# Kernel tuning notes

Hardware: AMD Instinct MI355X
Metric: run time of the kernel (lower is better)

## Reference

```python
import jax, jax.numpy as jnp
import numpy as np

T = 3
R = 0.05  # threshold on SQUARED distance (as in the source: dis < r)
N, M = 4, 384

_PSPEC = [("hW1", (3, 64)), ("hb1", (64,)), ("hW2", (64, 128)), ("hb2", (128,)), ("hW3", (128, 3)), ("hb3", (3,)),
          ("fW1", (6, 64)), ("fb1", (64,)), ("fW2", (64, 128)), ("fb2", (128,)), ("fW3", (128, 128)), ("fb3", (128,)),
          ("gW1", (128, 64)), ("gb1", (64,)), ("gW2", (64, 32)), ("gb2", (32,)), ("gW3", (32, 3)), ("gb3", (3,))]


def setup_inputs() -> dict:
    key = jax.random.key(0)
    inp = {"x": jax.random.uniform(key, (N, M, 3), jnp.float32)}
    for i, (name, shp) in enumerate(_PSPEC):
        k = jax.random.fold_in(key, i + 1)
        scale = 1.0 / np.sqrt(shp[0]) if len(shp) == 2 else 0.01
        inp[name] = jax.random.normal(k, (T,) + shp, jnp.float32) * jnp.float32(scale)
    return inp


def _mlp(x, W1, b1, W2, b2, W3, b3, final_relu):
    h = jax.nn.relu(x @ W1 + b1)
    h = jax.nn.relu(h @ W2 + b2)
    o = h @ W3 + b3
    return jax.nn.relu(o) if final_relu else o


def _forward(x, hW1, hb1, hW2, hb2, hW3, hb3, fW1, fb1, fW2, fb2, fW3, fb3, gW1, gb1, gW2, gb2, gW3, gb3):
    n, m, _ = x.shape
    diff = x[:, :, None, :] - x[:, None, :, :]              # (N,M,M,3)
    adj = jnp.sum(diff * diff, axis=-1) < R                 # (N,M,M) squared-dist ball
    state = x
    for t in range(T):
        # NOTE on MLP_h / delta: in the source, xj and xi inside getTimeEdges are
        # IDENTICAL broadcasts of xi_delta (both x.unsqueeze(-2).repeat over dim -2),
        # so xi[adj] = xj[adj] - xi[adj] == 0 everywhere. The relative-position
        # slot is therefore exactly zeros and delta = MLP_h(state) never affects
        # the output (and receives zero gradient in torch as well).
        rel = jnp.zeros((n, m, m, 3), x.dtype)
        # state[n,i,j,:] = state[n,j,:] where adj[n,i,j], else 0
        sfull = jnp.where(adj[..., None], state[:, None, :, :], 0.0)  # (N,M,M,3)
        eij = jnp.concatenate([rel, sfull], axis=-1)                   # (N,M,M,6)
        e = _mlp(eij, fW1[t], fb1[t], fW2[t], fb2[t], fW3[t], fb3[t], True)  # (N,M,M,128)
        e = jnp.where(adj[..., None], e, 0.0)
        agg = jnp.max(e, axis=2)                                       # max over neighbors j -> (N,M,128)
        state = _mlp(agg, gW1[t], gb1[t], gW2[t], gb2[t], gW3[t], gb3[t], True) + state
    return state


def reference(x, hW1, hb1, hW2, hb2, hW3, hb3, fW1, fb1, fW2, fb2, fW3, fb3, gW1, gb1, gW2, gb2, gW3, gb3):
    return _forward(x, hW1, hb1, hW2, hb2, hW3, hb3, fW1, fb1, fW2, fb2, fW3, fb3, gW1, gb1, gW2, gb2, gW3, gb3)
```

## Files before the change

### kernel.cpp

```cpp
#include <hip/hip_runtime.h>

#define MNODES 384
#define RTHRESH 0.05f
#define NWAVES 6
#define NBLOCKS 256


__device__ __forceinline__ void phi_stage(
    const float* __restrict__ fW1, const float* __restrict__ fb1,
    const float* __restrict__ fW2, const float* __restrict__ fb2,
    const float* __restrict__ fW3, const float* __restrict__ fb3,
    float s0, float s1, float s2, int lane,
    float* __restrict__ H1, float* __restrict__ H2,
    float* __restrict__ phidst )
{
    float v = fb1[lane];
    v = fmaf(s0, fW1[3 * 64 + lane], v);
    v = fmaf(s1, fW1[4 * 64 + lane], v);
    v = fmaf(s2, fW1[5 * 64 + lane], v);
    H1[lane] = fmaxf(v, 0.0f);

    const int l2 = lane * 2;
    const float2 b2 = *(const float2*)(fb2 + l2);
    float a0 = b2.x, a1 = b2.y;
#pragma unroll 16
    for (int c = 0; c < 64; ++c) {
        const float h = H1[c];
        const float2 w = *(const float2*)(fW2 + c * 128 + l2);
        a0 = fmaf(h, w.x, a0);
        a1 = fmaf(h, w.y, a1);
    }
    H2[l2] = fmaxf(a0, 0.0f);
    H2[l2 + 1] = fmaxf(a1, 0.0f);

    const float2 b3 = *(const float2*)(fb3 + l2);
    float c0 = b3.x, c1 = b3.y;
#pragma unroll 16
    for (int c = 0; c < 128; ++c) {
        const float h = H2[c];
        const float2 w = *(const float2*)(fW3 + c * 128 + l2);
        c0 = fmaf(h, w.x, c0);
        c1 = fmaf(h, w.y, c1);
    }
    *(float2*)(phidst + l2) = make_float2(fmaxf(c0, 0.0f), fmaxf(c1, 0.0f));
}

__global__ __launch_bounds__(384) void adj_phi0_kernel(
    const float* __restrict__ x,
    const float* __restrict__ fW1, const float* __restrict__ fb1,
    const float* __restrict__ fW2, const float* __restrict__ fb2,
    const float* __restrict__ fW3, const float* __restrict__ fb3,
    int* __restrict__ cnt, unsigned short* __restrict__ lists,
    float* __restrict__ phiA)
{
    __shared__ float xs[MNODES * 3];
    __shared__ float work[NWAVES][192];
    const int tid = threadIdx.x;
    const int wv = tid >> 6, lane = tid & 63;
    const int node = blockIdx.x * NWAVES + wv;
    const int n = blockIdx.x >> 6;
    const int i = node - n * MNODES;

    for (int idx = tid; idx < MNODES * 3; idx += 384)
        xs[idx] = x[n * MNODES * 3 + idx];
    __syncthreads();

    const float s0 = xs[i * 3], s1 = xs[i * 3 + 1], s2 = xs[i * 3 + 2];
    unsigned short* ml = lists + (size_t)node * MNODES;
    int nc = 0;
#pragma unroll
    for (int rep = 0; rep < 6; ++rep) {
        const int j = rep * 64 + lane;
        float dx = xs[j * 3] - s0;
        float dy = xs[j * 3 + 1] - s1;
        float dz = xs[j * 3 + 2] - s2;
        float d2 = __fadd_rn(__fadd_rn(__fmul_rn(dx, dx), __fmul_rn(dy, dy)),
                             __fmul_rn(dz, dz));
        const bool a = d2 < RTHRESH;
        const unsigned long long m = __ballot(a);
        if (a) ml[nc + __popcll(m & ((1ull << lane) - 1ull))] = (unsigned short)j;
        nc += (int)__popcll(m);
    }
    if (lane == 0) cnt[node] = nc;

    phi_stage(fW1, fb1, fW2, fb2, fW3, fb3, s0, s1, s2, lane,
              &work[wv][0], &work[wv][64], phiA + (size_t)node * 128);
}

__global__ __launch_bounds__(384) void step_kernel(
    const float* __restrict__ phisrc, float* __restrict__ phidst,
    const int* __restrict__ cnt, const unsigned short* __restrict__ lists,
    const float* __restrict__ statesrc, float* __restrict__ statedst,
    const float* __restrict__ gW1, const float* __restrict__ gb1,
    const float* __restrict__ gW2, const float* __restrict__ gb2,
    const float* __restrict__ gW3, const float* __restrict__ gb3,
    const float* __restrict__ fW1n, const float* __restrict__ fb1n,
    const float* __restrict__ fW2n, const float* __restrict__ fb2n,
    const float* __restrict__ fW3n, const float* __restrict__ fb3n,
    int do_phi)
{
    __shared__ float work[NWAVES][224];
    const int tid = threadIdx.x;
    const int wv = tid >> 6, lane = tid & 63;
    const int node = __builtin_amdgcn_readfirstlane(blockIdx.x * NWAVES + wv);
    const int nbase = (blockIdx.x >> 6) * MNODES;
    const int nc = cnt[node];
    const unsigned short* ml = lists + (size_t)node * MNODES;
    const float* pb = phisrc + (size_t)nbase * 128;
    float* const aggL = &work[wv][0];
    float* const h1L  = &work[wv][128];
    float* const h2L  = &work[wv][192];
    const int l2 = lane * 2;

    float m[8], p[8];
#pragma unroll
    for (int k = 0; k < 8; ++k) { m[k] = 0.0f; p[k] = 0.0f; }
    const int last = nc - 1;
    for (int jj = 0; jj < nc; jj += 8) {
        const float* r[8];
#pragma unroll
        for (int k = 0; k < 8; ++k) {
            const int jc = jj + k;
            const int j = ml[jc < last ? jc : last];
            r[k] = pb + (size_t)j * 128;
        }
#pragma unroll
        for (int k = 0; k < 8; ++k) {
            const float2 v = *(const float2*)(r[k] + l2);
            m[k] = fmaxf(m[k], v.x);
            p[k] = fmaxf(p[k], v.y);
        }
    }
    aggL[l2] = fmaxf(fmaxf(fmaxf(m[0], m[1]), fmaxf(m[2], m[3])),
                     fmaxf(fmaxf(m[4], m[5]), fmaxf(m[6], m[7])));
    aggL[l2 + 1] = fmaxf(fmaxf(fmaxf(p[0], p[1]), fmaxf(p[2], p[3])),
                         fmaxf(fmaxf(p[4], p[5]), fmaxf(p[6], p[7])));

    float h = gb1[lane];
#pragma unroll 16
    for (int c = 0; c < 128; ++c) h = fmaf(aggL[c], gW1[c * 64 + lane], h);
    h1L[lane] = fmaxf(h, 0.0f);
    if (lane < 32) {
        float v2 = gb2[lane];
#pragma unroll 16
        for (int k = 0; k < 64; ++k) v2 = fmaf(h1L[k], gW2[k * 32 + lane], v2);
        h2L[lane] = fmaxf(v2, 0.0f);
    }
    float sv = 0.0f;
    if (lane < 3) sv = statesrc[node * 3 + lane];
    float ns = 0.0f;
    if (lane < 3) {
        float v3 = gb3[lane];
#pragma unroll
        for (int q = 0; q < 32; ++q) v3 = fmaf(h2L[q], gW3[q * 3 + lane], v3);
        ns = fmaxf(v3, 0.0f) + sv;
        statedst[node * 3 + lane] = ns;
    }
    if (do_phi) {
        const float s0 = __shfl(ns, 0), s1 = __shfl(ns, 1), s2 = __shfl(ns, 2);
        phi_stage(fW1n, fb1n, fW2n, fb2n, fW3n, fb3n, s0, s1, s2, lane,
                  &work[wv][0], &work[wv][64], phidst + (size_t)node * 128);
    }
}

extern "C" void kernel_launch(void* const* d_in, const int* in_sizes, int n_in,
                              void* d_out, int out_size, void* d_ws, size_t ws_size,
                              hipStream_t stream) {
    const float* x   = (const float*)d_in[0];
    const float* fW1 = (const float*)d_in[7];
    const float* fb1 = (const float*)d_in[8];
    const float* fW2 = (const float*)d_in[9];
    const float* fb2 = (const float*)d_in[10];
    const float* fW3 = (const float*)d_in[11];
    const float* fb3 = (const float*)d_in[12];
    const float* gW1 = (const float*)d_in[13];
    const float* gb1 = (const float*)d_in[14];
    const float* gW2 = (const float*)d_in[15];
    const float* gb2 = (const float*)d_in[16];
    const float* gW3 = (const float*)d_in[17];
    const float* gb3 = (const float*)d_in[18];

    char* ws = (char*)d_ws;
    unsigned short* lists = (unsigned short*)(ws + 0);
    int* cnt              = (int*)(ws + 1179648);
    float* phiA           = (float*)(ws + 1185792);
    float* phiB           = (float*)(ws + 1972224);
    float* stateA         = (float*)(ws + 2758656);
    float* stateB         = (float*)(ws + 2777088);
    float* outp           = (float*)d_out;

    adj_phi0_kernel<<<NBLOCKS, 64 * NWAVES, 0, stream>>>(
        x, fW1, fb1, fW2, fb2, fW3, fb3, cnt, lists, phiA);
    step_kernel<<<NBLOCKS, 64 * NWAVES, 0, stream>>>(
        phiA, phiB, cnt, lists, x, stateA,
        gW1, gb1, gW2, gb2, gW3, gb3,
        fW1 + 384, fb1 + 64, fW2 + 8192, fb2 + 128,
        fW3 + 16384, fb3 + 128, 1);
    step_kernel<<<NBLOCKS, 64 * NWAVES, 0, stream>>>(
        phiB, phiA, cnt, lists, stateA, stateB,
        gW1 + 8192, gb1 + 64, gW2 + 2048, gb2 + 32,
        gW3 + 96, gb3 + 3,
        fW1 + 768, fb1 + 128, fW2 + 16384, fb2 + 256,
        fW3 + 32768, fb3 + 256, 1);
    step_kernel<<<NBLOCKS, 64 * NWAVES, 0, stream>>>(
        phiA, phiB, cnt, lists, stateB, outp,
        gW1 + 16384, gb1 + 128, gW2 + 4096, gb2 + 64,
        gW3 + 192, gb3 + 6,
        fW1, fb1, fW2, fb2, fW3, fb3, 0);
}
```

Baseline: 139.9 us.

## Split each node across two waves with one node per block

Instead of one wave per node with six nodes per block, each block now handles a single node using two waves. The adjacency scan, the neighbour max-gather and the phi MLP layers are split across the two waves by column or by half of the candidate range. Neighbour lists are kept as two half-lists with per-half counts. The aim is more blocks and more parallel work per node, which should cut per-node latency on the serial MLP chains. The cost is block-wide syncs and duplicated g-MLP work in both waves.

Result: no change. 140.1 us (+0.1%).

```diff
diff --git a/kernel.cpp b/kernel.cpp
--- a/kernel.cpp
+++ b/kernel.cpp
@@ -2,75 +2,38 @@
 
 #define MNODES 384
 #define RTHRESH 0.05f
-#define NWAVES 6
-#define NBLOCKS 256
-
-
-__device__ __forceinline__ void phi_stage(
-    const float* __restrict__ fW1, const float* __restrict__ fb1,
-    const float* __restrict__ fW2, const float* __restrict__ fb2,
-    const float* __restrict__ fW3, const float* __restrict__ fb3,
-    float s0, float s1, float s2, int lane,
-    float* __restrict__ H1, float* __restrict__ H2,
-    float* __restrict__ phidst )
-{
-    float v = fb1[lane];
-    v = fmaf(s0, fW1[3 * 64 + lane], v);
-    v = fmaf(s1, fW1[4 * 64 + lane], v);
-    v = fmaf(s2, fW1[5 * 64 + lane], v);
-    H1[lane] = fmaxf(v, 0.0f);
-
-    const int l2 = lane * 2;
-    const float2 b2 = *(const float2*)(fb2 + l2);
-    float a0 = b2.x, a1 = b2.y;
-#pragma unroll 16
-    for (int c = 0; c < 64; ++c) {
-        const float h = H1[c];
-        const float2 w = *(const float2*)(fW2 + c * 128 + l2);
-        a0 = fmaf(h, w.x, a0);
-        a1 = fmaf(h, w.y, a1);
-    }
-    H2[l2] = fmaxf(a0, 0.0f);
-    H2[l2 + 1] = fmaxf(a1, 0.0f);
-
-    const float2 b3 = *(const float2*)(fb3 + l2);
-    float c0 = b3.x, c1 = b3.y;
-#pragma unroll 16
-    for (int c = 0; c < 128; ++c) {
-        const float h = H2[c];
-        const float2 w = *(const float2*)(fW3 + c * 128 + l2);
-        c0 = fmaf(h, w.x, c0);
-        c1 = fmaf(h, w.y, c1);
-    }
-    *(float2*)(phidst + l2) = make_float2(fmaxf(c0, 0.0f), fmaxf(c1, 0.0f));
-}
-
-__global__ __launch_bounds__(384) void adj_phi0_kernel(
+#define NBLK 1536
+#define NTHR 128
+
+
+__global__ __launch_bounds__(NTHR) void adj_phi0_kernel(
     const float* __restrict__ x,
     const float* __restrict__ fW1, const float* __restrict__ fb1,
     const float* __restrict__ fW2, const float* __restrict__ fb2,
     const float* __restrict__ fW3, const float* __restrict__ fb3,
-    int* __restrict__ cnt, unsigned short* __restrict__ lists,
+    unsigned short* __restrict__ cnt2, unsigned short* __restrict__ lists,
     float* __restrict__ phiA)
 {
     __shared__ float xs[MNODES * 3];
-    __shared__ float work[NWAVES][192];
+    __shared__ float H1L[2][64];
+    __shared__ float H2[128];
     const int tid = threadIdx.x;
     const int wv = tid >> 6, lane = tid & 63;
-    const int node = blockIdx.x * NWAVES + wv;
-    const int n = blockIdx.x >> 6;
+    const int node = blockIdx.x;
+    const int n = node / MNODES;
     const int i = node - n * MNODES;
 
-    for (int idx = tid; idx < MNODES * 3; idx += 384)
+    for (int idx = tid; idx < MNODES * 3; idx += NTHR)
         xs[idx] = x[n * MNODES * 3 + idx];
     __syncthreads();
 
     const float s0 = xs[i * 3], s1 = xs[i * 3 + 1], s2 = xs[i * 3 + 2];
-    unsigned short* ml = lists + (size_t)node * MNODES;
+
+    unsigned short* ml = lists + (size_t)node * MNODES + wv * 192;
     int nc = 0;
 #pragma unroll
-    for (int rep = 0; rep < 6; ++rep) {
-        const int j = rep * 64 + lane;
+    for (int rep = 0; rep < 3; ++rep) {
+        const int j = wv * 192 + rep * 64 + lane;
         float dx = xs[j * 3] - s0;
         float dy = xs[j * 3 + 1] - s1;
         float dz = xs[j * 3 + 2] - s2;
@@ -81,15 +44,32 @@
         if (a) ml[nc + __popcll(m & ((1ull << lane) - 1ull))] = (unsigned short)j;
         nc += (int)__popcll(m);
     }
-    if (lane == 0) cnt[node] = nc;
-
-    phi_stage(fW1, fb1, fW2, fb2, fW3, fb3, s0, s1, s2, lane,
-              &work[wv][0], &work[wv][64], phiA + (size_t)node * 128);
+    if (lane == 0) cnt2[node * 2 + wv] = (unsigned short)nc;
+
+    float v = fb1[lane];
+    v = fmaf(s0, fW1[3 * 64 + lane], v);
+    v = fmaf(s1, fW1[4 * 64 + lane], v);
+    v = fmaf(s2, fW1[5 * 64 + lane], v);
+    H1L[wv][lane] = fmaxf(v, 0.0f);
+
+    const int col = wv * 64 + lane;
+    float a2 = fb2[col];
+#pragma unroll 16
+    for (int c = 0; c < 64; ++c)
+        a2 = fmaf(H1L[wv][c], fW2[c * 128 + col], a2);
+    H2[col] = fmaxf(a2, 0.0f);
+    __syncthreads();
+
+    float c0 = fb3[col];
+#pragma unroll 16
+    for (int c = 0; c < 128; ++c)
+        c0 = fmaf(H2[c], fW3[c * 128 + col], c0);
+    phiA[(size_t)node * 128 + col] = fmaxf(c0, 0.0f);
 }
 
-__global__ __launch_bounds__(384) void step_kernel(
+__global__ __launch_bounds__(NTHR) void step_kernel(
     const float* __restrict__ phisrc, float* __restrict__ phidst,
-    const int* __restrict__ cnt, const unsigned short* __restrict__ lists,
+    const unsigned short* __restrict__ cnt2, const unsigned short* __restrict__ lists,
     const float* __restrict__ statesrc, float* __restrict__ statedst,
     const float* __restrict__ gW1, const float* __restrict__ gb1,
     const float* __restrict__ gW2, const float* __restrict__ gb2,
@@ -99,67 +79,83 @@
     const float* __restrict__ fW3n, const float* __restrict__ fb3n,
     int do_phi)
 {
-    __shared__ float work[NWAVES][224];
+    __shared__ float aggL[128];
+    __shared__ float H2[128];
+    __shared__ float H1L[2][64];
+    __shared__ float h1L[2][64];
+    __shared__ float h2L[2][32];
     const int tid = threadIdx.x;
     const int wv = tid >> 6, lane = tid & 63;
-    const int node = __builtin_amdgcn_readfirstlane(blockIdx.x * NWAVES + wv);
-    const int nbase = (blockIdx.x >> 6) * MNODES;
-    const int nc = cnt[node];
+    const int node = blockIdx.x;
+    const int n = node / MNODES;
+    const int nbase = n * MNODES;
+    const int s0c = cnt2[node * 2 + 0];
+    const int s1c = cnt2[node * 2 + 1];
+    const int nc = s0c + s1c;
     const unsigned short* ml = lists + (size_t)node * MNODES;
     const float* pb = phisrc + (size_t)nbase * 128;
-    float* const aggL = &work[wv][0];
-    float* const h1L  = &work[wv][128];
-    float* const h2L  = &work[wv][192];
-    const int l2 = lane * 2;
-
-    float m[8], p[8];
-#pragma unroll
-    for (int k = 0; k < 8; ++k) { m[k] = 0.0f; p[k] = 0.0f; }
+    const int col = wv * 64 + lane;
+
+    float m[8];
+#pragma unroll
+    for (int k = 0; k < 8; ++k) m[k] = 0.0f;
     const int last = nc - 1;
     for (int jj = 0; jj < nc; jj += 8) {
         const float* r[8];
 #pragma unroll
         for (int k = 0; k < 8; ++k) {
-            const int jc = jj + k;
-            const int j = ml[jc < last ? jc : last];
-            r[k] = pb + (size_t)j * 128;
+            int jc = jj + k;
+            jc = jc < last ? jc : last;
+            const int idx = jc < s0c ? jc : 192 + (jc - s0c);
+            r[k] = pb + (size_t)ml[idx] * 128;
         }
 #pragma unroll
-        for (int k = 0; k < 8; ++k) {
-            const float2 v = *(const float2*)(r[k] + l2);
-            m[k] = fmaxf(m[k], v.x);
-            p[k] = fmaxf(p[k], v.y);
-        }
-    }
-    aggL[l2] = fmaxf(fmaxf(fmaxf(m[0], m[1]), fmaxf(m[2], m[3])),
-                     fmaxf(fmaxf(m[4], m[5]), fmaxf(m[6], m[7])));
-    aggL[l2 + 1] = fmaxf(fmaxf(fmaxf(p[0], p[1]), fmaxf(p[2], p[3])),
-                         fmaxf(fmaxf(p[4], p[5]), fmaxf(p[6], p[7])));
+        for (int k = 0; k < 8; ++k) m[k] = fmaxf(m[k], r[k][col]);
+    }
+    aggL[col] = fmaxf(fmaxf(fmaxf(m[0], m[1]), fmaxf(m[2], m[3])),
+                      fmaxf(fmaxf(m[4], m[5]), fmaxf(m[6], m[7])));
+    __syncthreads();
 
     float h = gb1[lane];
 #pragma unroll 16
     for (int c = 0; c < 128; ++c) h = fmaf(aggL[c], gW1[c * 64 + lane], h);
-    h1L[lane] = fmaxf(h, 0.0f);
+    h1L[wv][lane] = fmaxf(h, 0.0f);
     if (lane < 32) {
         float v2 = gb2[lane];
 #pragma unroll 16
-        for (int k = 0; k < 64; ++k) v2 = fmaf(h1L[k], gW2[k * 32 + lane], v2);
-        h2L[lane] = fmaxf(v2, 0.0f);
-    }
-    float sv = 0.0f;
-    if (lane < 3) sv = statesrc[node * 3 + lane];
+        for (int k = 0; k < 64; ++k) v2 = fmaf(h1L[wv][k], gW2[k * 32 + lane], v2);
+        h2L[wv][lane] = fmaxf(v2, 0.0f);
+    }
     float ns = 0.0f;
     if (lane < 3) {
+        const float sv = statesrc[node * 3 + lane];
         float v3 = gb3[lane];
 #pragma unroll
-        for (int q = 0; q < 32; ++q) v3 = fmaf(h2L[q], gW3[q * 3 + lane], v3);
+        for (int q = 0; q < 32; ++q) v3 = fmaf(h2L[wv][q], gW3[q * 3 + lane], v3);
         ns = fmaxf(v3, 0.0f) + sv;
-        statedst[node * 3 + lane] = ns;
-    }
+        if (wv == 0) statedst[node * 3 + lane] = ns;
+    }
+
     if (do_phi) {
-        const float s0 = __shfl(ns, 0), s1 = __shfl(ns, 1), s2 = __shfl(ns, 2);
-        phi_stage(fW1n, fb1n, fW2n, fb2n, fW3n, fb3n, s0, s1, s2, lane,
-                  &work[wv][0], &work[wv][64], phidst + (size_t)node * 128);
+        const float t0 = __shfl(ns, 0), t1 = __shfl(ns, 1), t2 = __shfl(ns, 2);
+        float v = fb1n[lane];
+        v = fmaf(t0, fW1n[3 * 64 + lane], v);
+        v = fmaf(t1, fW1n[4 * 64 + lane], v);
+        v = fmaf(t2, fW1n[5 * 64 + lane], v);
+        H1L[wv][lane] = fmaxf(v, 0.0f);
+
+        float a2 = fb2n[col];
+#pragma unroll 16
+        for (int c = 0; c < 64; ++c)
+            a2 = fmaf(H1L[wv][c], fW2n[c * 128 + col], a2);
+        H2[col] = fmaxf(a2, 0.0f);
+        __syncthreads();
+
+        float c0 = fb3n[col];
+#pragma unroll 16
+        for (int c = 0; c < 128; ++c)
+            c0 = fmaf(H2[c], fW3n[c * 128 + col], c0);
+        phidst[(size_t)node * 128 + col] = fmaxf(c0, 0.0f);
     }
 }
 
@@ -182,28 +178,28 @@
 
     char* ws = (char*)d_ws;
     unsigned short* lists = (unsigned short*)(ws + 0);
-    int* cnt              = (int*)(ws + 1179648);
+    unsigned short* cnt2  = (unsigned short*)(ws + 1179648);
     float* phiA           = (float*)(ws + 1185792);
     float* phiB           = (float*)(ws + 1972224);
     float* stateA         = (float*)(ws + 2758656);
     float* stateB         = (float*)(ws + 2777088);
     float* outp           = (float*)d_out;
 
-    adj_phi0_kernel<<<NBLOCKS, 64 * NWAVES, 0, stream>>>(
-        x, fW1, fb1, fW2, fb2, fW3, fb3, cnt, lists, phiA);
-    step_kernel<<<NBLOCKS, 64 * NWAVES, 0, stream>>>(
-        phiA, phiB, cnt, lists, x, stateA,
+    adj_phi0_kernel<<<NBLK, NTHR, 0, stream>>>(
+        x, fW1, fb1, fW2, fb2, fW3, fb3, cnt2, lists, phiA);
+    step_kernel<<<NBLK, NTHR, 0, stream>>>(
+        phiA, phiB, cnt2, lists, x, stateA,
         gW1, gb1, gW2, gb2, gW3, gb3,
         fW1 + 384, fb1 + 64, fW2 + 8192, fb2 + 128,
         fW3 + 16384, fb3 + 128, 1);
-    step_kernel<<<NBLOCKS, 64 * NWAVES, 0, stream>>>(
-        phiB, phiA, cnt, lists, stateA, stateB,
+    step_kernel<<<NBLK, NTHR, 0, stream>>>(
+        phiB, phiA, cnt2, lists, stateA, stateB,
         gW1 + 8192, gb1 + 64, gW2 + 2048, gb2 + 32,
         gW3 + 96, gb3 + 3,
         fW1 + 768, fb1 + 128, fW2 + 16384, fb2 + 256,
         fW3 + 32768, fb3 + 256, 1);
-    step_kernel<<<NBLOCKS, 64 * NWAVES, 0, stream>>>(
-        phiA, phiB, cnt, lists, stateB, outp,
+    step_kernel<<<NBLK, NTHR, 0, stream>>>(
+        phiA, phiB, cnt2, lists, stateB, outp,
         gW1 + 16384, gb1 + 128, gW2 + 4096, gb2 + 64,
         gW3 + 192, gb3 + 6,
         fW1, fb1, fW2, fb2, fW3, fb3, 0);
```

## Stage phi layer-3 weights in LDS and switch to 4-wave blocks

Applied to the files above, without the earlier changes.

Step kernels now copy the 128x128 fW3 weight matrix into shared memory once per block and read it from LDS in the final phi layer, instead of each wave streaming it from global/L2. Blocks shrink from 6 to 4 waves and the grid grows to 384 blocks. Per-lane access changes from float2 pairs to two strided scalar elements (lane, lane+64). The 64KB LDS staging cuts occupancy and adds a block-wide barrier, and each block reloads the weights for only four nodes.

Result: faster. 136.6 us (-2.4%).

```diff
diff --git a/kernel.cpp b/kernel.cpp
--- a/kernel.cpp
+++ b/kernel.cpp
@@ -2,8 +2,6 @@
 
 #define MNODES 384
 #define RTHRESH 0.05f
-#define NWAVES 6
-#define NBLOCKS 256
 
 
 __device__ __forceinline__ void phi_stage(
@@ -19,33 +17,27 @@
     v = fmaf(s1, fW1[4 * 64 + lane], v);
     v = fmaf(s2, fW1[5 * 64 + lane], v);
     H1[lane] = fmaxf(v, 0.0f);
-
-    const int l2 = lane * 2;
-    const float2 b2 = *(const float2*)(fb2 + l2);
-    float a0 = b2.x, a1 = b2.y;
+    float a0 = fb2[lane], a1 = fb2[lane + 64];
 #pragma unroll 16
     for (int c = 0; c < 64; ++c) {
         const float h = H1[c];
-        const float2 w = *(const float2*)(fW2 + c * 128 + l2);
-        a0 = fmaf(h, w.x, a0);
-        a1 = fmaf(h, w.y, a1);
-    }
-    H2[l2] = fmaxf(a0, 0.0f);
-    H2[l2 + 1] = fmaxf(a1, 0.0f);
-
-    const float2 b3 = *(const float2*)(fb3 + l2);
-    float c0 = b3.x, c1 = b3.y;
+        a0 = fmaf(h, fW2[c * 128 + lane], a0);
+        a1 = fmaf(h, fW2[c * 128 + lane + 64], a1);
+    }
+    H2[lane] = fmaxf(a0, 0.0f);
+    H2[lane + 64] = fmaxf(a1, 0.0f);
+    float c0 = fb3[lane], c1 = fb3[lane + 64];
 #pragma unroll 16
     for (int c = 0; c < 128; ++c) {
         const float h = H2[c];
-        const float2 w = *(const float2*)(fW3 + c * 128 + l2);
-        c0 = fmaf(h, w.x, c0);
-        c1 = fmaf(h, w.y, c1);
-    }
-    *(float2*)(phidst + l2) = make_float2(fmaxf(c0, 0.0f), fmaxf(c1, 0.0f));
-}
-
-__global__ __launch_bounds__(384) void adj_phi0_kernel(
+        c0 = fmaf(h, fW3[c * 128 + lane], c0);
+        c1 = fmaf(h, fW3[c * 128 + lane + 64], c1);
+    }
+    phidst[lane] = fmaxf(c0, 0.0f);
+    phidst[lane + 64] = fmaxf(c1, 0.0f);
+}
+
+__global__ __launch_bounds__(256) void adj_phi0_kernel(
     const float* __restrict__ x,
     const float* __restrict__ fW1, const float* __restrict__ fb1,
     const float* __restrict__ fW2, const float* __restrict__ fb2,
@@ -54,14 +46,14 @@
     float* __restrict__ phiA)
 {
     __shared__ float xs[MNODES * 3];
-    __shared__ float work[NWAVES][192];
+    __shared__ float work[4][192];
     const int tid = threadIdx.x;
     const int wv = tid >> 6, lane = tid & 63;
-    const int node = blockIdx.x * NWAVES + wv;
-    const int n = blockIdx.x >> 6;
+    const int node = blockIdx.x * 4 + wv;
+    const int n = blockIdx.x / 96;
     const int i = node - n * MNODES;
 
-    for (int idx = tid; idx < MNODES * 3; idx += 384)
+    for (int idx = tid; idx < MNODES * 3; idx += 256)
         xs[idx] = x[n * MNODES * 3 + idx];
     __syncthreads();
 
@@ -87,7 +79,7 @@
               &work[wv][0], &work[wv][64], phiA + (size_t)node * 128);
 }
 
-__global__ __launch_bounds__(384) void step_kernel(
+__global__ __launch_bounds__(256) void step_kernel(
     const float* __restrict__ phisrc, float* __restrict__ phidst,
     const int* __restrict__ cnt, const unsigned short* __restrict__ lists,
     const float* __restrict__ statesrc, float* __restrict__ statedst,
@@ -99,18 +91,27 @@
     const float* __restrict__ fW3n, const float* __restrict__ fb3n,
     int do_phi)
 {
-    __shared__ float work[NWAVES][224];
+    __shared__ float work[4][224];
+    __shared__ float sW3[128 * 128];
     const int tid = threadIdx.x;
     const int wv = tid >> 6, lane = tid & 63;
-    const int node = __builtin_amdgcn_readfirstlane(blockIdx.x * NWAVES + wv);
-    const int nbase = (blockIdx.x >> 6) * MNODES;
+    const int node = __builtin_amdgcn_readfirstlane(blockIdx.x * 4 + wv);
+    const int nbase = (blockIdx.x / 96) * MNODES;
+
+    if (do_phi) {
+        const float4* src = (const float4*)fW3n;
+        float4* dst = (float4*)sW3;
+#pragma unroll 8
+        for (int k = 0; k < 16; ++k)
+            dst[tid + k * 256] = src[tid + k * 256];
+    }
+
     const int nc = cnt[node];
     const unsigned short* ml = lists + (size_t)node * MNODES;
     const float* pb = phisrc + (size_t)nbase * 128;
     float* const aggL = &work[wv][0];
     float* const h1L  = &work[wv][128];
     float* const h2L  = &work[wv][192];
-    const int l2 = lane * 2;
 
     float m[8], p[8];
 #pragma unroll
@@ -126,15 +127,14 @@
         }
 #pragma unroll
         for (int k = 0; k < 8; ++k) {
-            const float2 v = *(const float2*)(r[k] + l2);
-            m[k] = fmaxf(m[k], v.x);
-            p[k] = fmaxf(p[k], v.y);
-        }
-    }
-    aggL[l2] = fmaxf(fmaxf(fmaxf(m[0], m[1]), fmaxf(m[2], m[3])),
-                     fmaxf(fmaxf(m[4], m[5]), fmaxf(m[6], m[7])));
-    aggL[l2 + 1] = fmaxf(fmaxf(fmaxf(p[0], p[1]), fmaxf(p[2], p[3])),
-                         fmaxf(fmaxf(p[4], p[5]), fmaxf(p[6], p[7])));
+            m[k] = fmaxf(m[k], r[k][lane]);
+            p[k] = fmaxf(p[k], r[k][lane + 64]);
+        }
+    }
+    aggL[lane] = fmaxf(fmaxf(fmaxf(m[0], m[1]), fmaxf(m[2], m[3])),
+                       fmaxf(fmaxf(m[4], m[5]), fmaxf(m[6], m[7])));
+    aggL[lane + 64] = fmaxf(fmaxf(fmaxf(p[0], p[1]), fmaxf(p[2], p[3])),
+                            fmaxf(fmaxf(p[4], p[5]), fmaxf(p[6], p[7])));
 
     float h = gb1[lane];
 #pragma unroll 16
@@ -158,8 +158,32 @@
     }
     if (do_phi) {
         const float s0 = __shfl(ns, 0), s1 = __shfl(ns, 1), s2 = __shfl(ns, 2);
-        phi_stage(fW1n, fb1n, fW2n, fb2n, fW3n, fb3n, s0, s1, s2, lane,
-                  &work[wv][0], &work[wv][64], phidst + (size_t)node * 128);
+        float* const H1 = &work[wv][0];
+        float* const H2 = &work[wv][64];
+        float v = fb1n[lane];
+        v = fmaf(s0, fW1n[3 * 64 + lane], v);
+        v = fmaf(s1, fW1n[4 * 64 + lane], v);
+        v = fmaf(s2, fW1n[5 * 64 + lane], v);
+        H1[lane] = fmaxf(v, 0.0f);
+        float a0 = fb2n[lane], a1 = fb2n[lane + 64];
+#pragma unroll 16
+        for (int c = 0; c < 64; ++c) {
+            const float hh = H1[c];
+            a0 = fmaf(hh, fW2n[c * 128 + lane], a0);
+            a1 = fmaf(hh, fW2n[c * 128 + lane + 64], a1);
+        }
+        H2[lane] = fmaxf(a0, 0.0f);
+        H2[lane + 64] = fmaxf(a1, 0.0f);
+        __syncthreads();
+        float c0 = fb3n[lane], c1 = fb3n[lane + 64];
+#pragma unroll 16
+        for (int c = 0; c < 128; ++c) {
+            const float hh = H2[c];
+            c0 = fmaf(hh, sW3[c * 128 + lane], c0);
+            c1 = fmaf(hh, sW3[c * 128 + lane + 64], c1);
+        }
+        phidst[(size_t)node * 128 + lane] = fmaxf(c0, 0.0f);
+        phidst[(size_t)node * 128 + lane + 64] = fmaxf(c1, 0.0f);
     }
 }
 
@@ -189,22 +213,19 @@
     float* stateB         = (float*)(ws + 2777088);
     float* outp           = (float*)d_out;
 
-    adj_phi0_kernel<<<NBLOCKS, 64 * NWAVES, 0, stream>>>(
-        x, fW1, fb1, fW2, fb2, fW3, fb3, cnt, lists, phiA);
-    step_kernel<<<NBLOCKS, 64 * NWAVES, 0, stream>>>(
-        phiA, phiB, cnt, lists, x, stateA,
-        gW1, gb1, gW2, gb2, gW3, gb3,
-        fW1 + 384, fb1 + 64, fW2 + 8192, fb2 + 128,
-        fW3 + 16384, fb3 + 128, 1);
-    step_kernel<<<NBLOCKS, 64 * NWAVES, 0, stream>>>(
-        phiB, phiA, cnt, lists, stateA, stateB,
-        gW1 + 8192, gb1 + 64, gW2 + 2048, gb2 + 32,
-        gW3 + 96, gb3 + 3,
-        fW1 + 768, fb1 + 128, fW2 + 16384, fb2 + 256,
-        fW3 + 32768, fb3 + 256, 1);
-    step_kernel<<<NBLOCKS, 64 * NWAVES, 0, stream>>>(
-        phiA, phiB, cnt, lists, stateB, outp,
-        gW1 + 16384, gb1 + 128, gW2 + 4096, gb2 + 64,
-        gW3 + 192, gb3 + 6,
-        fW1, fb1, fW2, fb2, fW3, fb3, 0);
-}
+    adj_phi0_kernel<<<384, 256, 0, stream>>>(x, fW1, fb1, fW2, fb2, fW3, fb3,
+                                             cnt, lists, phiA);
+    step_kernel<<<384, 256, 0, stream>>>(phiA, phiB, cnt, lists, x, stateA,
+                                         gW1, gb1, gW2, gb2, gW3, gb3,
+                                         fW1 + 384, fb1 + 64, fW2 + 8192, fb2 + 128,
+                                         fW3 + 16384, fb3 + 128, 1);
+    step_kernel<<<384, 256, 0, stream>>>(phiB, phiA, cnt, lists, stateA, stateB,
+                                         gW1 + 8192, gb1 + 64, gW2 + 2048, gb2 + 32,
+                                         gW3 + 96, gb3 + 3,
+                                         fW1 + 768, fb1 + 128, fW2 + 16384, fb2 + 256,
+                                         fW3 + 32768, fb3 + 256, 1);
+    step_kernel<<<384, 256, 0, stream>>>(phiA, phiB, cnt, lists, stateB, outp,
+                                         gW1 + 16384, gb1 + 128, gW2 + 4096, gb2 + 64,
+                                         gW3 + 192, gb3 + 6,
+                                         fW1, fb1, fW2, fb2, fW3, fb3, 0);
+}
```
